# Optimization experiments

Hardware: AMD Instinct MI355X
Metric: run time of the kernel (lower is better)

Reference implementation:

```python
import jax, jax.numpy as jnp
import numpy as np

B, H, I = 16, 1024, 512


def setup_inputs() -> dict:
    key = jax.random.key(0)
    ks = jax.random.split(key, 20)
    W = 0.05  # small weight scale to avoid gate saturation (mimics uniform Xavier init)
    inp = {
        "x": jax.random.normal(ks[0], (B, I), jnp.float32),
        "w_ix": jax.random.normal(ks[1], (H, I), jnp.float32) * W,
        "w_ih": jax.random.normal(ks[2], (H, H), jnp.float32) * W,
        "b_i": jnp.ones((H,), jnp.float32),
        "w_fx": jax.random.normal(ks[3], (H, I), jnp.float32) * W,
        "w_fh": jax.random.normal(ks[4], (H, H), jnp.float32) * W,
        "b_f": jnp.ones((H,), jnp.float32),
        "w_ox": jax.random.normal(ks[5], (H, I), jnp.float32) * W,
        "w_oh": jax.random.normal(ks[6], (H, H), jnp.float32) * W,
        "b_o": jnp.ones((H,), jnp.float32),
        "w_cx": jax.random.normal(ks[7], (H, I), jnp.float32) * W,
        "w_ch": jax.random.normal(ks[8], (H, H), jnp.float32) * W,
        "b_c": jnp.zeros((H,), jnp.float32),
        "h_last": jax.random.normal(ks[9], (B, H), jnp.float32) * 0.1,
        "c_last": jax.random.normal(ks[10], (B, H), jnp.float32) * 0.1,
        "e_w_ix": jax.random.normal(ks[11], (B, H, I), jnp.float32) * 0.01,
        "e_w_ih": jax.random.normal(ks[12], (B, H, H), jnp.float32) * 0.01,
        "e_b_i": jax.random.normal(ks[13], (B, H), jnp.float32) * 0.01,
        "e_w_fx": jax.random.normal(ks[14], (B, H, I), jnp.float32) * 0.01,
        "e_w_fh": jax.random.normal(ks[15], (B, H, H), jnp.float32) * 0.01,
        "e_b_f": jax.random.normal(ks[16], (B, H), jnp.float32) * 0.01,
        "e_w_cx": jax.random.normal(ks[17], (B, H, I), jnp.float32) * 0.01,
        "e_w_ch": jax.random.normal(ks[18], (B, H, H), jnp.float32) * 0.01,
        "e_b_c": jax.random.normal(ks[19], (B, H), jnp.float32) * 0.01,
    }
    return inp


def reference(x, w_ix, w_ih, b_i, w_fx, w_fh, b_f, w_ox, w_oh, b_o,
              w_cx, w_ch, b_c, h_last, c_last,
              e_w_ix, e_w_ih, e_b_i, e_w_fx, e_w_fh, e_b_f,
              e_w_cx, e_w_ch, e_b_c):
    # Gate GEMMs  [B,H]
    i = jax.nn.sigmoid(x @ w_ix.T + h_last @ w_ih.T + b_i)
    f = jax.nn.sigmoid(x @ w_fx.T + h_last @ w_fh.T + b_f)
    o = jax.nn.sigmoid(x @ w_ox.T + h_last @ w_oh.T + b_o)
    c_hat = jnp.tanh(x @ w_cx.T + h_last @ w_ch.T + b_c)
    c = f * c_last + i * c_hat
    h = o * c

    # Gate derivatives
    di = i * (1.0 - i)
    df = f * (1.0 - f)
    dc_hat = 1.0 - c_hat * c_hat
    # Broadcast helpers: *_j -> [B,H,1], *_i -> [B,1,dim]
    f_j = f[:, :, None]
    x_i = x[:, None, :]
    h_i = h_last[:, None, :]
    a_i = (di * c_hat)[:, :, None]   # di_j * c_hat_j
    a_f = (df * c_last)[:, :, None]  # df_j * c_last_j
    a_c = (dc_hat * i)[:, :, None]   # dc_hat_j * i_j

    # Eligibility trace updates (outer-product broadcasts)
    new_e_w_ih = e_w_ih * f_j + a_i * h_i
    new_e_w_ix = e_w_ix * f_j + a_i * x_i
    new_e_b_i = e_b_i * f + di * c_hat
    new_e_w_fh = e_w_fh * f_j + a_f * h_i
    new_e_w_fx = e_w_fx * f_j + a_f * x_i
    new_e_b_f = e_b_f * f + df * c_last
    new_e_w_ch = e_w_ch * f_j + a_c * h_i
    new_e_w_cx = e_w_cx * f_j + a_c * x_i
    new_e_b_c = e_b_c * f + dc_hat * i

    return (h, c,
            new_e_w_ix, new_e_w_ih, new_e_b_i,
            new_e_w_fx, new_e_w_fh, new_e_b_f,
            new_e_w_cx, new_e_w_ch, new_e_b_c)
```

## Files before the change

### kernel.cpp

```cpp
#include <hip/hip_runtime.h>
#include <stdint.h>

#define BB 16
#define HH 1024
#define II 512

#define OFF_H    0L
#define OFF_C    16384L
#define OFF_EWIX 32768L
#define OFF_EWIH 8421376L
#define OFF_EBI  25198592L
#define OFF_EWFX 25214976L
#define OFF_EWFH 33603584L
#define OFF_EBF  50380800L
#define OFF_EWCX 50397184L
#define OFF_EWCH 58785792L
#define OFF_EBC  75563008L

typedef float f4 __attribute__((ext_vector_type(4)));

__device__ __forceinline__ void load8f(const float* __restrict__ p, float* o) {
    float4 a = *(const float4*)p;
    float4 b = *(const float4*)(p + 4);
    o[0] = a.x; o[1] = a.y; o[2] = a.z; o[3] = a.w;
    o[4] = b.x; o[5] = b.y; o[6] = b.z; o[7] = b.w;
}

__global__ __launch_bounds__(64) void k_gates(
    const float* __restrict__ x,
    const float* __restrict__ w_ix, const float* __restrict__ w_ih, const float* __restrict__ b_i,
    const float* __restrict__ w_fx, const float* __restrict__ w_fh, const float* __restrict__ b_f,
    const float* __restrict__ w_ox, const float* __restrict__ w_oh, const float* __restrict__ b_o,
    const float* __restrict__ w_cx, const float* __restrict__ w_ch, const float* __restrict__ b_c,
    const float* __restrict__ h_last, const float* __restrict__ c_last,
    const float* __restrict__ e_b_i, const float* __restrict__ e_b_f, const float* __restrict__ e_b_c,
    float* __restrict__ out, float* __restrict__ ws)
{
    const int h = blockIdx.x;
    const int lane = threadIdx.x;

    float acc0[BB], acc1[BB], acc2[BB], acc3[BB];
    #pragma unroll
    for (int b = 0; b < BB; b++) { acc0[b] = 0.f; acc1[b] = 0.f; acc2[b] = 0.f; acc3[b] = 0.f; }

    {
        const int k = lane * 8;
        float wi[8], wf[8], wo[8], wc[8];
        load8f(w_ix + (size_t)h * II + k, wi);
        load8f(w_fx + (size_t)h * II + k, wf);
        load8f(w_ox + (size_t)h * II + k, wo);
        load8f(w_cx + (size_t)h * II + k, wc);
        #pragma unroll
        for (int b = 0; b < BB; b++) {
            float xv[8];
            load8f(x + b * II + k, xv);
            #pragma unroll
            for (int e = 0; e < 8; e++) {
                acc0[b] += wi[e] * xv[e];
                acc1[b] += wf[e] * xv[e];
                acc2[b] += wo[e] * xv[e];
                acc3[b] += wc[e] * xv[e];
            }
        }
    }
    #pragma unroll
    for (int c0 = 0; c0 < 2; c0++) {
        const int k = c0 * 512 + lane * 8;
        float wi[8], wf[8], wo[8], wc[8];
        load8f(w_ih + (size_t)h * HH + k, wi);
        load8f(w_fh + (size_t)h * HH + k, wf);
        load8f(w_oh + (size_t)h * HH + k, wo);
        load8f(w_ch + (size_t)h * HH + k, wc);
        #pragma unroll
        for (int b = 0; b < BB; b++) {
            float hv[8];
            load8f(h_last + b * HH + k, hv);
            #pragma unroll
            for (int e = 0; e < 8; e++) {
                acc0[b] += wi[e] * hv[e];
                acc1[b] += wf[e] * hv[e];
                acc2[b] += wo[e] * hv[e];
                acc3[b] += wc[e] * hv[e];
            }
        }
    }

    __shared__ float red[64][65];
    #pragma unroll
    for (int b = 0; b < BB; b++) {
        red[lane][b]      = acc0[b];
        red[lane][16 + b] = acc1[b];
        red[lane][32 + b] = acc2[b];
        red[lane][48 + b] = acc3[b];
    }
    __syncthreads();
    float pre = 0.f;
    #pragma unroll
    for (int l = 0; l < 64; l++) pre += red[l][lane];

    const int bb = lane & 15;
    const float pi0 = __shfl(pre, bb,      64);
    const float pf0 = __shfl(pre, bb + 16, 64);
    const float po0 = __shfl(pre, bb + 32, 64);
    const float pc0 = __shfl(pre, bb + 48, 64);

    if (lane < BB) {
        const int b = lane;
        const int idx = b * HH + h;
        const float pi = pi0 + b_i[h];
        const float pf = pf0 + b_f[h];
        const float po = po0 + b_o[h];
        const float pc = pc0 + b_c[h];
        const float ig = 1.f / (1.f + __expf(-pi));
        const float fg = 1.f / (1.f + __expf(-pf));
        const float og = 1.f / (1.f + __expf(-po));
        const float chat = tanhf(pc);
        const float cl = c_last[idx];
        const float cnew = fg * cl + ig * chat;
        const float hnew = og * cnew;
        const float di = ig * (1.f - ig);
        const float df = fg * (1.f - fg);
        const float dch = 1.f - chat * chat;
        const float ai = di * chat;
        const float af = df * cl;
        const float ac = dch * ig;

        out[OFF_H   + idx] = hnew;
        out[OFF_C   + idx] = cnew;
        out[OFF_EBI + idx] = e_b_i[idx] * fg + ai;
        out[OFF_EBF + idx] = e_b_f[idx] * fg + af;
        out[OFF_EBC + idx] = e_b_c[idx] * fg + ac;

        ws[idx]          = fg;
        ws[16384 + idx]  = ai;
        ws[32768 + idx]  = af;
        ws[49152 + idx]  = ac;
    }
}

__global__ __launch_bounds__(256) void k_trace(
    const float* __restrict__ x, const float* __restrict__ h_last,
    const float* __restrict__ e_ix, const float* __restrict__ e_ih,
    const float* __restrict__ e_fx, const float* __restrict__ e_fh,
    const float* __restrict__ e_cx, const float* __restrict__ e_ch,
    const float* __restrict__ ws, float* __restrict__ out)
{
    const int t = blockIdx.y;
    const int is_h = t & 1;
    const int qrl = 7 + is_h;

    const float* e_in; long ooff;
    switch (t) {
        case 0:  e_in = e_ix; ooff = OFF_EWIX; break;
        case 1:  e_in = e_ih; ooff = OFF_EWIH; break;
        case 2:  e_in = e_fx; ooff = OFF_EWFX; break;
        case 3:  e_in = e_fh; ooff = OFF_EWFH; break;
        case 4:  e_in = e_cx; ooff = OFF_EWCX; break;
        default: e_in = e_ch; ooff = OFF_EWCH; break;
    }
    const float* src = is_h ? h_last : x;
    const int a_base = ((t >> 1) + 1) << 14;

    const f4* e4 = (const f4*)e_in;
    const f4* s4 = (const f4*)src;
    f4* o4 = (f4*)(out + ooff);

    const int tiles = 1 + is_h;
    for (int it = 0; it < tiles; ++it) {
        const int tile = ((int)blockIdx.x + (it << 11)) << 10;
        #pragma unroll
        for (int u = 0; u < 4; ++u) {
            const int q   = tile + (u << 8) + (int)threadIdx.x;
            const int row = q >> qrl;
            const int jq  = q & ((1 << qrl) - 1);
            const int b   = row >> 10;
            const float fl = ws[row];
            const float aa = ws[a_base + row];
            f4 ev = __builtin_nontemporal_load(e4 + q);
            f4 sv = s4[(b << qrl) + jq];
            f4 r;
            r[0] = ev[0] * fl + aa * sv[0];
            r[1] = ev[1] * fl + aa * sv[1];
            r[2] = ev[2] * fl + aa * sv[2];
            r[3] = ev[3] * fl + aa * sv[3];
            __builtin_nontemporal_store(r, o4 + q);
        }
    }
}

extern "C" void kernel_launch(void* const* d_in, const int* in_sizes, int n_in,
                              void* d_out, int out_size, void* d_ws, size_t ws_size,
                              hipStream_t stream) {
    const float* x      = (const float*)d_in[0];
    const float* w_ix   = (const float*)d_in[1];
    const float* w_ih   = (const float*)d_in[2];
    const float* b_i    = (const float*)d_in[3];
    const float* w_fx   = (const float*)d_in[4];
    const float* w_fh   = (const float*)d_in[5];
    const float* b_f    = (const float*)d_in[6];
    const float* w_ox   = (const float*)d_in[7];
    const float* w_oh   = (const float*)d_in[8];
    const float* b_o    = (const float*)d_in[9];
    const float* w_cx   = (const float*)d_in[10];
    const float* w_ch   = (const float*)d_in[11];
    const float* b_c    = (const float*)d_in[12];
    const float* h_last = (const float*)d_in[13];
    const float* c_last = (const float*)d_in[14];
    const float* e_ix   = (const float*)d_in[15];
    const float* e_ih   = (const float*)d_in[16];
    const float* e_b_i  = (const float*)d_in[17];
    const float* e_fx   = (const float*)d_in[18];
    const float* e_fh   = (const float*)d_in[19];
    const float* e_b_f  = (const float*)d_in[20];
    const float* e_cx   = (const float*)d_in[21];
    const float* e_ch   = (const float*)d_in[22];
    const float* e_b_c  = (const float*)d_in[23];
    float* out = (float*)d_out;
    float* ws  = (float*)d_ws;

    k_gates<<<dim3(HH), dim3(64), 0, stream>>>(
        x, w_ix, w_ih, b_i, w_fx, w_fh, b_f, w_ox, w_oh, b_o, w_cx, w_ch, b_c,
        h_last, c_last, e_b_i, e_b_f, e_b_c, out, ws);

    k_trace<<<dim3(2048, 6), dim3(256), 0, stream>>>(
        x, h_last, e_ix, e_ih, e_fx, e_fh, e_cx, e_ch, ws, out);
}
```

Before: 538.7 us.

## Split gate GEMV across four waves and flatten trace grid with batched loads

The gates kernel now runs 256 threads per hidden unit, one wave per gate, instead of one wave computing all four gates. This cuts per-thread register pressure and adds parallelism, and the reduction now goes through a shared-memory partial sum plus shuffles. The trace kernel uses a flat 1D grid that gives each block one 1024-element tile, with the H-sized traces scheduled first. Its loads are issued for all four elements before any compute, which exposes more memory-level parallelism in the bandwidth-bound streaming pass.

```diff
diff --git a/kernel.cpp b/kernel.cpp
--- a/kernel.cpp
+++ b/kernel.cpp
@@ -26,7 +26,7 @@
     o[4] = b.x; o[5] = b.y; o[6] = b.z; o[7] = b.w;
 }
 
-__global__ __launch_bounds__(64) void k_gates(
+__global__ __launch_bounds__(256) void k_gates(
     const float* __restrict__ x,
     const float* __restrict__ w_ix, const float* __restrict__ w_ih, const float* __restrict__ b_i,
     const float* __restrict__ w_fx, const float* __restrict__ w_fh, const float* __restrict__ b_f,
@@ -36,81 +36,71 @@
     const float* __restrict__ e_b_i, const float* __restrict__ e_b_f, const float* __restrict__ e_b_c,
     float* __restrict__ out, float* __restrict__ ws)
 {
-    const int h = blockIdx.x;
-    const int lane = threadIdx.x;
-
-    float acc0[BB], acc1[BB], acc2[BB], acc3[BB];
-    #pragma unroll
-    for (int b = 0; b < BB; b++) { acc0[b] = 0.f; acc1[b] = 0.f; acc2[b] = 0.f; acc3[b] = 0.f; }
+    const int h    = blockIdx.x;
+    const int wave = threadIdx.x >> 6;
+    const int lane = threadIdx.x & 63;
+
+    const float* wx; const float* wh;
+    switch (wave) {
+        case 0:  wx = w_ix; wh = w_ih; break;
+        case 1:  wx = w_fx; wh = w_fh; break;
+        case 2:  wx = w_ox; wh = w_oh; break;
+        default: wx = w_cx; wh = w_ch; break;
+    }
+
+    float acc[BB];
+    #pragma unroll
+    for (int b = 0; b < BB; b++) acc[b] = 0.f;
 
     {
         const int k = lane * 8;
-        float wi[8], wf[8], wo[8], wc[8];
-        load8f(w_ix + (size_t)h * II + k, wi);
-        load8f(w_fx + (size_t)h * II + k, wf);
-        load8f(w_ox + (size_t)h * II + k, wo);
-        load8f(w_cx + (size_t)h * II + k, wc);
+        float wv[8];
+        load8f(wx + (size_t)h * II + k, wv);
         #pragma unroll
         for (int b = 0; b < BB; b++) {
             float xv[8];
             load8f(x + b * II + k, xv);
             #pragma unroll
-            for (int e = 0; e < 8; e++) {
-                acc0[b] += wi[e] * xv[e];
-                acc1[b] += wf[e] * xv[e];
-                acc2[b] += wo[e] * xv[e];
-                acc3[b] += wc[e] * xv[e];
-            }
+            for (int e = 0; e < 8; e++) acc[b] += wv[e] * xv[e];
         }
     }
     #pragma unroll
     for (int c0 = 0; c0 < 2; c0++) {
         const int k = c0 * 512 + lane * 8;
-        float wi[8], wf[8], wo[8], wc[8];
-        load8f(w_ih + (size_t)h * HH + k, wi);
-        load8f(w_fh + (size_t)h * HH + k, wf);
-        load8f(w_oh + (size_t)h * HH + k, wo);
-        load8f(w_ch + (size_t)h * HH + k, wc);
+        float wv[8];
+        load8f(wh + (size_t)h * HH + k, wv);
         #pragma unroll
         for (int b = 0; b < BB; b++) {
             float hv[8];
             load8f(h_last + b * HH + k, hv);
             #pragma unroll
-            for (int e = 0; e < 8; e++) {
-                acc0[b] += wi[e] * hv[e];
-                acc1[b] += wf[e] * hv[e];
-                acc2[b] += wo[e] * hv[e];
-                acc3[b] += wc[e] * hv[e];
-            }
+            for (int e = 0; e < 8; e++) acc[b] += wv[e] * hv[e];
         }
     }
 
-    __shared__ float red[64][65];
-    #pragma unroll
-    for (int b = 0; b < BB; b++) {
-        red[lane][b]      = acc0[b];
-        red[lane][16 + b] = acc1[b];
-        red[lane][32 + b] = acc2[b];
-        red[lane][48 + b] = acc3[b];
-    }
+    __shared__ float red[4][64][17];
+    __shared__ float pre_s[4][16];
+    #pragma unroll
+    for (int b = 0; b < BB; b++) red[wave][lane][b] = acc[b];
     __syncthreads();
-    float pre = 0.f;
-    #pragma unroll
-    for (int l = 0; l < 64; l++) pre += red[l][lane];
-
+
+    const int q  = lane >> 4;
     const int bb = lane & 15;
-    const float pi0 = __shfl(pre, bb,      64);
-    const float pf0 = __shfl(pre, bb + 16, 64);
-    const float po0 = __shfl(pre, bb + 32, 64);
-    const float pc0 = __shfl(pre, bb + 48, 64);
-
-    if (lane < BB) {
-        const int b = lane;
+    float part = 0.f;
+    #pragma unroll
+    for (int i = 0; i < 16; i++) part += red[wave][q * 16 + i][bb];
+    part += __shfl_xor(part, 16, 64);
+    part += __shfl_xor(part, 32, 64);
+    if (lane < 16) pre_s[wave][lane] = part;
+    __syncthreads();
+
+    if (threadIdx.x < BB) {
+        const int b = threadIdx.x;
         const int idx = b * HH + h;
-        const float pi = pi0 + b_i[h];
-        const float pf = pf0 + b_f[h];
-        const float po = po0 + b_o[h];
-        const float pc = pc0 + b_c[h];
+        const float pi = pre_s[0][b] + b_i[h];
+        const float pf = pre_s[1][b] + b_f[h];
+        const float po = pre_s[2][b] + b_o[h];
+        const float pc = pre_s[3][b] + b_c[h];
         const float ig = 1.f / (1.f + __expf(-pi));
         const float fg = 1.f / (1.f + __expf(-pf));
         const float og = 1.f / (1.f + __expf(-po));
@@ -145,46 +135,53 @@
     const float* __restrict__ e_cx, const float* __restrict__ e_ch,
     const float* __restrict__ ws, float* __restrict__ out)
 {
-    const int t = blockIdx.y;
-    const int is_h = t & 1;
+    const int bid = (int)blockIdx.x;
+    int t, tile, is_h;
+    if (bid < 12288) { t = bid >> 12; tile = bid & 4095; is_h = 1; }
+    else { const int r = bid - 12288; t = 3 + (r >> 11); tile = r & 2047; is_h = 0; }
     const int qrl = 7 + is_h;
 
     const float* e_in; long ooff;
     switch (t) {
-        case 0:  e_in = e_ix; ooff = OFF_EWIX; break;
-        case 1:  e_in = e_ih; ooff = OFF_EWIH; break;
-        case 2:  e_in = e_fx; ooff = OFF_EWFX; break;
-        case 3:  e_in = e_fh; ooff = OFF_EWFH; break;
-        case 4:  e_in = e_cx; ooff = OFF_EWCX; break;
-        default: e_in = e_ch; ooff = OFF_EWCH; break;
+        case 0:  e_in = e_ih; ooff = OFF_EWIH; break;
+        case 1:  e_in = e_fh; ooff = OFF_EWFH; break;
+        case 2:  e_in = e_ch; ooff = OFF_EWCH; break;
+        case 3:  e_in = e_ix; ooff = OFF_EWIX; break;
+        case 4:  e_in = e_fx; ooff = OFF_EWFX; break;
+        default: e_in = e_cx; ooff = OFF_EWCX; break;
     }
     const float* src = is_h ? h_last : x;
-    const int a_base = ((t >> 1) + 1) << 14;
+    const int a_sel = (t < 3) ? t : (t - 3);
+    const int a_base = (a_sel + 1) << 14;
 
     const f4* e4 = (const f4*)e_in;
     const f4* s4 = (const f4*)src;
     f4* o4 = (f4*)(out + ooff);
 
-    const int tiles = 1 + is_h;
-    for (int it = 0; it < tiles; ++it) {
-        const int tile = ((int)blockIdx.x + (it << 11)) << 10;
-        #pragma unroll
-        for (int u = 0; u < 4; ++u) {
-            const int q   = tile + (u << 8) + (int)threadIdx.x;
-            const int row = q >> qrl;
-            const int jq  = q & ((1 << qrl) - 1);
-            const int b   = row >> 10;
-            const float fl = ws[row];
-            const float aa = ws[a_base + row];
-            f4 ev = __builtin_nontemporal_load(e4 + q);
-            f4 sv = s4[(b << qrl) + jq];
-            f4 r;
-            r[0] = ev[0] * fl + aa * sv[0];
-            r[1] = ev[1] * fl + aa * sv[1];
-            r[2] = ev[2] * fl + aa * sv[2];
-            r[3] = ev[3] * fl + aa * sv[3];
-            __builtin_nontemporal_store(r, o4 + q);
-        }
+    const int base = (tile << 10) + (int)threadIdx.x;
+
+    f4 ev[4], sv[4];
+    float fl[4], aa[4];
+    int q[4];
+    #pragma unroll
+    for (int u = 0; u < 4; ++u) {
+        q[u] = base + (u << 8);
+        const int row = q[u] >> qrl;
+        const int jq  = q[u] & ((1 << qrl) - 1);
+        const int b   = row >> 10;
+        ev[u] = __builtin_nontemporal_load(e4 + q[u]);
+        sv[u] = s4[(b << qrl) + jq];
+        fl[u] = ws[row];
+        aa[u] = ws[a_base + row];
+    }
+    #pragma unroll
+    for (int u = 0; u < 4; ++u) {
+        f4 r;
+        r[0] = ev[u][0] * fl[u] + aa[u] * sv[u][0];
+        r[1] = ev[u][1] * fl[u] + aa[u] * sv[u][1];
+        r[2] = ev[u][2] * fl[u] + aa[u] * sv[u][2];
+        r[3] = ev[u][3] * fl[u] + aa[u] * sv[u][3];
+        __builtin_nontemporal_store(r, o4 + q[u]);
     }
 }
 
@@ -218,10 +215,10 @@
     float* out = (float*)d_out;
     float* ws  = (float*)d_ws;
 
-    k_gates<<<dim3(HH), dim3(64), 0, stream>>>(
+    k_gates<<<dim3(HH), dim3(256), 0, stream>>>(
         x, w_ix, w_ih, b_i, w_fx, w_fh, b_f, w_ox, w_oh, b_o, w_cx, w_ch, b_c,
         h_last, c_last, e_b_i, e_b_f, e_b_c, out, ws);
 
-    k_trace<<<dim3(2048, 6), dim3(256), 0, stream>>>(
+    k_trace<<<dim3(18432), dim3(256), 0, stream>>>(
         x, h_last, e_ix, e_ih, e_fx, e_fh, e_cx, e_ch, ws, out);
 }
```

After: 539.8 us. Within noise of the previous version (+0.2%).
